# Optimization experiments

Hardware: AMD Instinct MI355X
Metric: run time of the kernel (lower is better)

## Reference

```python
import jax, jax.numpy as jnp
import numpy as np

EPS_RMS = 1e-6
Q_CLIP_MIN = 1e-5

def setup_inputs() -> dict:
    key = jax.random.key(0)
    k1, k2 = jax.random.split(key)
    x = jax.random.normal(k1, (1, 2048, 4096), dtype=jnp.float32)
    # kaiming_uniform-ish init for weight [in_features, out_features]
    fan_in = 4096
    bound = 1.0 / np.sqrt(fan_in)
    weight = jax.random.uniform(k2, (4096, 4096), dtype=jnp.float32, minval=-bound, maxval=bound)
    rms_weight = jnp.ones((4096,), dtype=jnp.float32)
    return {"x": x, "weight": weight, "rms_weight": rms_weight}

def reference(x, weight, rms_weight):
    # RMSNorm over last dim
    xn = x * jax.lax.rsqrt(jnp.mean(x * x, axis=-1, keepdims=True) + EPS_RMS) * rms_weight
    K = weight.shape[0]
    orig_shape = xn.shape
    x2 = xn.reshape(-1, K)  # [M, K]

    # per-tensor absmax int8 activation quantization
    a_scale = 127.0 / jnp.clip(jnp.max(jnp.abs(x2)), Q_CLIP_MIN)
    A_q = jnp.clip(jnp.round(x2 * a_scale), -128.0, 127.0)

    # absmean ternary weight quantization
    b_scale = 1.0 / jnp.clip(jnp.mean(jnp.abs(weight)), Q_CLIP_MIN)
    B_t = jnp.clip(jnp.round(weight * b_scale), -1.0, 1.0)

    # integer matmul + dequant: (A_q @ B_t) / (a_scale * b_scale)
    out = (A_q @ B_t) / (a_scale * b_scale)  # [M, N]
    return out.reshape(*orig_shape[:-1], weight.shape[1])
```

## Files before the change

### kernel.cpp

```cpp
#include <hip/hip_runtime.h>
#include <cstdint>

#define M_DIM 2048
#define K_DIM 4096
#define N_DIM 4096

#define BM 256
#define BN 128
#define BK 128
#define KT (K_DIM / BK)
#define A_TILE_BYTES (BM * BK)
#define B_TILE_BYTES (BN * BK)
#define TILE_BYTES (A_TILE_BYTES + B_TILE_BYTES)
#define NBUF 3
#define LDS_BYTES (NBUF * TILE_BYTES)

typedef __attribute__((ext_vector_type(4))) int i32x4;

__device__ __forceinline__ void gload_lds16(const void* g, void* l) {
  __builtin_amdgcn_global_load_lds(
      (__attribute__((address_space(1))) void*)(g),
      (__attribute__((address_space(3))) void*)(l), 16, 0, 0);
}

__global__ void fused_reduce_kernel(const float* __restrict__ x,
                                    const float* __restrict__ rw,
                                    const float* __restrict__ w,
                                    float* __restrict__ invrms,
                                    float* __restrict__ rowmax,
                                    double* __restrict__ partials) {
  const int tid = threadIdx.x;
  __shared__ double red[4];
  __shared__ float redf[4];
  __shared__ float sInv;

  if (blockIdx.x < 2048) {
    const int row = blockIdx.x;
    const float4* xr = (const float4*)(x + (size_t)row * K_DIM);
    const float4* wr = (const float4*)rw;
    float4 xv[4];
    double ss = 0.0;
#pragma unroll
    for (int i = 0; i < 4; i++) {
      xv[i] = xr[i * 256 + tid];
      ss += (double)xv[i].x * xv[i].x + (double)xv[i].y * xv[i].y +
            (double)xv[i].z * xv[i].z + (double)xv[i].w * xv[i].w;
    }
    for (int off = 32; off; off >>= 1) ss += __shfl_down(ss, off);
    if ((tid & 63) == 0) red[tid >> 6] = ss;
    __syncthreads();
    if (tid == 0) {
      double t = red[0] + red[1] + red[2] + red[3];
      sInv = (float)(1.0 / sqrt(t * (1.0 / (double)K_DIM) + 1e-6));
    }
    __syncthreads();
    const float inv = sInv;
    if (tid == 0) invrms[row] = inv;

    float amax = 0.f;
#pragma unroll
    for (int i = 0; i < 4; i++) {
      float4 wv = wr[i * 256 + tid];
      amax = fmaxf(amax, fabsf((xv[i].x * inv) * wv.x));
      amax = fmaxf(amax, fabsf((xv[i].y * inv) * wv.y));
      amax = fmaxf(amax, fabsf((xv[i].z * inv) * wv.z));
      amax = fmaxf(amax, fabsf((xv[i].w * inv) * wv.w));
    }
    for (int off = 32; off; off >>= 1) amax = fmaxf(amax, __shfl_down(amax, off));
    if ((tid & 63) == 0) redf[tid >> 6] = amax;
    __syncthreads();
    if (tid == 0)
      rowmax[row] = fmaxf(fmaxf(redf[0], redf[1]), fmaxf(redf[2], redf[3]));
  } else {
    const int bid = blockIdx.x - 2048;
    const float4* w4 = (const float4*)w;
    const size_t base = (size_t)bid * 2048;
    double s = 0.0;
#pragma unroll
    for (int i = 0; i < 8; i++) {
      float4 v = w4[base + i * 256 + tid];
      s += (double)((fabsf(v.x) + fabsf(v.y)) + (fabsf(v.z) + fabsf(v.w)));
    }
    for (int off = 32; off; off >>= 1) s += __shfl_down(s, off);
    if ((tid & 63) == 0) red[tid >> 6] = s;
    __syncthreads();
    if (tid == 0) partials[bid] = red[0] + red[1] + red[2] + red[3];
  }
}

__global__ void scales_kernel(const float* __restrict__ rowmax,
                              const double* __restrict__ partials,
                              float* __restrict__ scales) {
  const int tid = threadIdx.x;
  float m = 0.f;
  double s = 0.0;
#pragma unroll
  for (int i = 0; i < 8; i++) {
    m = fmaxf(m, rowmax[i * 256 + tid]);
    s += partials[i * 256 + tid];
  }
  for (int off = 32; off; off >>= 1) {
    m = fmaxf(m, __shfl_down(m, off));
    s += __shfl_down(s, off);
  }
  __shared__ float redf[4];
  __shared__ double red[4];
  if ((tid & 63) == 0) { redf[tid >> 6] = m; red[tid >> 6] = s; }
  __syncthreads();
  if (tid == 0) {
    float amax = fmaxf(fmaxf(redf[0], redf[1]), fmaxf(redf[2], redf[3]));
    double wsum = red[0] + red[1] + red[2] + red[3];
    float as = 127.0f / fmaxf(amax, 1e-5f);
    float mean_f = (float)(wsum * (1.0 / 16777216.0));
    float bs = 1.0f / fmaxf(mean_f, 1e-5f);
    scales[0] = as;
    scales[1] = bs;
    scales[2] = 1.0f / (as * bs);
  }
}

__global__ void fused_quant_kernel(const float* __restrict__ x,
                                   const float* __restrict__ rw,
                                   const float* __restrict__ invrms,
                                   const float* __restrict__ scales,
                                   const float* __restrict__ w,
                                   char* __restrict__ Aq,
                                   char* __restrict__ Bt) {
  const int tid = threadIdx.x;
  if (blockIdx.x < 2048) {
    const int row = blockIdx.x;
    const float inv = invrms[row];
    const float as = scales[0];
    const float4* xr = (const float4*)(x + (size_t)row * K_DIM);
    const float4* wr = (const float4*)rw;
    union { char c[16]; int4 v; } o;
#pragma unroll
    for (int i = 0; i < 4; i++) {
      float4 xv = xr[tid * 4 + i];
      float4 wv = wr[tid * 4 + i];
      float t0 = (xv.x * inv) * wv.x;
      float t1 = (xv.y * inv) * wv.y;
      float t2 = (xv.z * inv) * wv.z;
      float t3 = (xv.w * inv) * wv.w;
      o.c[i * 4 + 0] = (char)(int)fminf(fmaxf(rintf(t0 * as), -128.f), 127.f);
      o.c[i * 4 + 1] = (char)(int)fminf(fmaxf(rintf(t1 * as), -128.f), 127.f);
      o.c[i * 4 + 2] = (char)(int)fminf(fmaxf(rintf(t2 * as), -128.f), 127.f);
      o.c[i * 4 + 3] = (char)(int)fminf(fmaxf(rintf(t3 * as), -128.f), 127.f);
    }
    *(int4*)(Aq + (size_t)row * K_DIM + tid * 16) = o.v;
  } else {
    __shared__ float lds[64][68];
    const int tile = blockIdx.x - 2048;
    const int n0 = (tile & 63) * 64;
    const int k0 = (tile >> 6) * 64;
    const float bs = scales[1];
#pragma unroll
    for (int i = 0; i < 4; i++) {
      const int id = i * 256 + tid;
      const int r = id >> 4;
      const int c4 = (id & 15) * 4;
      float4 v = *(const float4*)(w + (size_t)(k0 + r) * N_DIM + n0 + c4);
      lds[c4 + 0][r] = fminf(fmaxf(rintf(v.x * bs), -1.f), 1.f);
      lds[c4 + 1][r] = fminf(fmaxf(rintf(v.y * bs), -1.f), 1.f);
      lds[c4 + 2][r] = fminf(fmaxf(rintf(v.z * bs), -1.f), 1.f);
      lds[c4 + 3][r] = fminf(fmaxf(rintf(v.w * bs), -1.f), 1.f);
    }
    __syncthreads();
    const int rn = tid >> 2;
    const int kg = (tid & 3) * 16;
    union { char c[16]; int4 v; } o;
#pragma unroll
    for (int j = 0; j < 16; j++) o.c[j] = (char)(int)lds[rn][kg + j];
    *(int4*)(Bt + (size_t)(n0 + rn) * K_DIM + k0 + kg) = o.v;
  }
}

__global__ void __launch_bounds__(512, 2)
gemm_kernel(const char* __restrict__ Aq, const char* __restrict__ Bt,
            float* __restrict__ out, const float* __restrict__ scales) {
  extern __shared__ char lds[];
  const int tid = threadIdx.x;
  const int lane = tid & 63;
  const int wave = tid >> 6;
  const int wm = wave >> 1;
  const int wn = wave & 1;
  const int brow = blockIdx.y * BM;
  const int bcol = blockIdx.x * BN;

  i32x4 acc[4][4];
#pragma unroll
  for (int m = 0; m < 4; m++)
#pragma unroll
    for (int n = 0; n < 4; n++) acc[m][n] = {0, 0, 0, 0};

  const int sRow8 = lane >> 3;
  const int srcColB = ((lane & 7) ^ sRow8) * 16;

#define STAGE_A(kt, bi, s)                                                        \
  gload_lds16(Aq + (size_t)(brow + (s)*64 + wave * 8 + sRow8) * K_DIM +           \
                  (kt)*BK + srcColB,                                              \
              lds + (bi)*TILE_BYTES + (s)*8192 + wave * 1024 + lane * 16)
#define STAGE_B(kt, bi, s)                                                        \
  gload_lds16(Bt + (size_t)(bcol + (s)*64 + wave * 8 + sRow8) * K_DIM +           \
                  (kt)*BK + srcColB,                                              \
              lds + (bi)*TILE_BYTES + A_TILE_BYTES + (s)*8192 + wave * 1024 +     \
                  lane * 16)

  STAGE_A(0, 0, 0); STAGE_A(0, 0, 1); STAGE_A(0, 0, 2); STAGE_A(0, 0, 3);
  STAGE_B(0, 0, 0); STAGE_B(0, 0, 1);
  STAGE_A(1, 1, 0); STAGE_A(1, 1, 1); STAGE_A(1, 1, 2); STAGE_A(1, 1, 3);
  STAGE_B(1, 1, 0); STAGE_B(1, 1, 1);
  asm volatile("s_waitcnt vmcnt(6)" ::: "memory");
  __builtin_amdgcn_s_barrier();

  const int aBase = (wm * 64 + (lane & 15)) * BK;
  const int bBase = (wn * 64 + (lane & 15)) * BK;
  const int swz0 = ((0 * 4 + (lane >> 4)) ^ (lane & 7)) * 16;
  const int swz1 = ((1 * 4 + (lane >> 4)) ^ (lane & 7)) * 16;

  int bi = 0;
  for (int t = 0; t < KT; ++t) {
    const char* bufA = lds + bi * TILE_BYTES;
    const char* bufB = bufA + A_TILE_BYTES;
    const int si = (bi + 2 >= NBUF) ? bi + 2 - NBUF : bi + 2;
    const bool doStage = (t + 2) < KT;

    i32x4 a0_[4], a1_[4], b0_[4], b1_[4];

#pragma unroll
    for (int s = 0; s < 2; s++) {
      a0_[s * 2 + 0] = *(const i32x4*)(bufA + aBase + s * 2048 + swz0);
      a0_[s * 2 + 1] = *(const i32x4*)(bufA + aBase + s * 2048 + swz1);
      b0_[s * 2 + 0] = *(const i32x4*)(bufB + bBase + s * 2048 + swz0);
      b0_[s * 2 + 1] = *(const i32x4*)(bufB + bBase + s * 2048 + swz1);
    }
    if (doStage) { STAGE_A(t + 2, si, 0); STAGE_A(t + 2, si, 1); }
    __builtin_amdgcn_s_barrier();
    asm volatile("s_waitcnt lgkmcnt(0)" ::: "memory");
    __builtin_amdgcn_sched_barrier(0);
    __builtin_amdgcn_s_setprio(1);
#pragma unroll
    for (int mi = 0; mi < 2; mi++)
#pragma unroll
      for (int ni = 0; ni < 2; ni++)
#pragma unroll
        for (int ks = 0; ks < 2; ks++)
          acc[mi][ni] = __builtin_amdgcn_mfma_i32_16x16x64_i8(
              a0_[mi * 2 + ks], b0_[ni * 2 + ks], acc[mi][ni], 0, 0, 0);
    __builtin_amdgcn_s_setprio(0);
    __builtin_amdgcn_s_barrier();

#pragma unroll
    for (int s = 0; s < 2; s++) {
      b1_[s * 2 + 0] = *(const i32x4*)(bufB + bBase + (s + 2) * 2048 + swz0);
      b1_[s * 2 + 1] = *(const i32x4*)(bufB + bBase + (s + 2) * 2048 + swz1);
    }
    if (doStage) { STAGE_A(t + 2, si, 2); STAGE_A(t + 2, si, 3); }
    __builtin_amdgcn_s_barrier();
    asm volatile("s_waitcnt lgkmcnt(0)" ::: "memory");
    __builtin_amdgcn_sched_barrier(0);
    __builtin_amdgcn_s_setprio(1);
#pragma unroll
    for (int mi = 0; mi < 2; mi++)
#pragma unroll
      for (int ni = 0; ni < 2; ni++)
#pragma unroll
        for (int ks = 0; ks < 2; ks++)
          acc[mi][ni + 2] = __builtin_amdgcn_mfma_i32_16x16x64_i8(
              a0_[mi * 2 + ks], b1_[ni * 2 + ks], acc[mi][ni + 2], 0, 0, 0);
    __builtin_amdgcn_s_setprio(0);
    __builtin_amdgcn_s_barrier();

#pragma unroll
    for (int s = 0; s < 2; s++) {
      a1_[s * 2 + 0] = *(const i32x4*)(bufA + aBase + (s + 2) * 2048 + swz0);
      a1_[s * 2 + 1] = *(const i32x4*)(bufA + aBase + (s + 2) * 2048 + swz1);
    }
    if (doStage) { STAGE_B(t + 2, si, 0); STAGE_B(t + 2, si, 1); }
    __builtin_amdgcn_s_barrier();
    asm volatile("s_waitcnt lgkmcnt(0)" ::: "memory");
    __builtin_amdgcn_sched_barrier(0);
    __builtin_amdgcn_s_setprio(1);
#pragma unroll
    for (int mi = 0; mi < 2; mi++)
#pragma unroll
      for (int ni = 0; ni < 2; ni++)
#pragma unroll
        for (int ks = 0; ks < 2; ks++)
          acc[mi + 2][ni] = __builtin_amdgcn_mfma_i32_16x16x64_i8(
              a1_[mi * 2 + ks], b0_[ni * 2 + ks], acc[mi + 2][ni], 0, 0, 0);
    __builtin_amdgcn_s_setprio(0);
    __builtin_amdgcn_s_barrier();

    __builtin_amdgcn_s_setprio(1);
#pragma unroll
    for (int mi = 0; mi < 2; mi++)
#pragma unroll
      for (int ni = 0; ni < 2; ni++)
#pragma unroll
        for (int ks = 0; ks < 2; ks++)
          acc[mi + 2][ni + 2] = __builtin_amdgcn_mfma_i32_16x16x64_i8(
              a1_[mi * 2 + ks], b1_[ni * 2 + ks], acc[mi + 2][ni + 2], 0, 0, 0);
    __builtin_amdgcn_s_setprio(0);
    if (t < KT - 1) {
      asm volatile("s_waitcnt vmcnt(6)" ::: "memory");
    } else {
      asm volatile("s_waitcnt vmcnt(0)" ::: "memory");
    }
    __builtin_amdgcn_s_barrier();

    bi = (bi + 1 >= NBUF) ? 0 : bi + 1;
  }
#undef STAGE_A
#undef STAGE_B

  const float dq = scales[2];
#pragma unroll
  for (int m = 0; m < 4; m++) {
#pragma unroll
    for (int n = 0; n < 4; n++) {
      const int row = wm * 64 + m * 16 + (lane >> 4) * 4;
      const int col = wn * 64 + n * 16 + (lane & 15);
#pragma unroll
      for (int j = 0; j < 4; j++) {
        out[(size_t)(brow + row + j) * N_DIM + bcol + col] = (float)acc[m][n][j] * dq;
      }
    }
  }
}

extern "C" void kernel_launch(void* const* d_in, const int* in_sizes, int n_in,
                              void* d_out, int out_size, void* d_ws, size_t ws_size,
                              hipStream_t stream) {
  const float* x      = (const float*)d_in[0];
  const float* weight = (const float*)d_in[1];
  const float* rms_w  = (const float*)d_in[2];
  float* out = (float*)d_out;

  uint8_t* ws = (uint8_t*)d_ws;
  float* scales    = (float*)(ws + 0);
  float* invrms    = (float*)(ws + 64);
  float* rowmax    = (float*)(ws + 64 + 8192);
  double* partials = (double*)(ws + 64 + 16384);
  char* Aq = (char*)(ws + 65536);
  char* Bt = (char*)(ws + 65536 + (size_t)M_DIM * K_DIM);

  (void)hipFuncSetAttribute((const void*)gemm_kernel,
                            hipFuncAttributeMaxDynamicSharedMemorySize, LDS_BYTES);

  fused_reduce_kernel<<<4096, 256, 0, stream>>>(x, rms_w, weight, invrms, rowmax, partials);
  scales_kernel<<<1, 256, 0, stream>>>(rowmax, partials, scales);
  fused_quant_kernel<<<6144, 256, 0, stream>>>(x, rms_w, invrms, scales, weight, Aq, Bt);
  gemm_kernel<<<dim3(N_DIM / BN, M_DIM / BM), 512, LDS_BYTES, stream>>>(Aq, Bt, out, scales);
}
```

Before: 77.32 us.

## Cut per-iteration barriers to one and overlap LDS reads with MFMA via partial lgkmcnt waits

Restructures the int8 GEMM main loop so each K-step has a single vmcnt wait plus workgroup barrier at the top, replacing the many intra-iteration s_barriers. LDS fragment loads for the next MFMA group are issued before the current group runs, and partial lgkmcnt(4) waits let MFMAs start while later loads are still in flight. Global-to-LDS staging is regrouped as 3+3 issues instead of 2+2+2. The aim is to remove barrier stalls and expose more load/compute overlap. The cost is tighter reliance on the triple-buffer distance for correctness, since fewer barriers separate staging writes from reads of other buffers.

```diff
diff --git a/kernel.cpp b/kernel.cpp
--- a/kernel.cpp
+++ b/kernel.cpp
@@ -210,8 +210,6 @@
   STAGE_B(0, 0, 0); STAGE_B(0, 0, 1);
   STAGE_A(1, 1, 0); STAGE_A(1, 1, 1); STAGE_A(1, 1, 2); STAGE_A(1, 1, 3);
   STAGE_B(1, 1, 0); STAGE_B(1, 1, 1);
-  asm volatile("s_waitcnt vmcnt(6)" ::: "memory");
-  __builtin_amdgcn_s_barrier();
 
   const int aBase = (wm * 64 + (lane & 15)) * BK;
   const int bBase = (wn * 64 + (lane & 15)) * BK;
@@ -220,23 +218,37 @@
 
   int bi = 0;
   for (int t = 0; t < KT; ++t) {
+    if (t < KT - 1) {
+      asm volatile("s_waitcnt vmcnt(6)" ::: "memory");
+    } else {
+      asm volatile("s_waitcnt vmcnt(0)" ::: "memory");
+    }
+    __builtin_amdgcn_s_barrier();
+    __builtin_amdgcn_sched_barrier(0);
+
     const char* bufA = lds + bi * TILE_BYTES;
     const char* bufB = bufA + A_TILE_BYTES;
     const int si = (bi + 2 >= NBUF) ? bi + 2 - NBUF : bi + 2;
     const bool doStage = (t + 2) < KT;
 
-    i32x4 a0_[4], a1_[4], b0_[4], b1_[4];
+    i32x4 a0[4], a1[4], b0[4], b1[4];
 
 #pragma unroll
     for (int s = 0; s < 2; s++) {
-      a0_[s * 2 + 0] = *(const i32x4*)(bufA + aBase + s * 2048 + swz0);
-      a0_[s * 2 + 1] = *(const i32x4*)(bufA + aBase + s * 2048 + swz1);
-      b0_[s * 2 + 0] = *(const i32x4*)(bufB + bBase + s * 2048 + swz0);
-      b0_[s * 2 + 1] = *(const i32x4*)(bufB + bBase + s * 2048 + swz1);
-    }
-    if (doStage) { STAGE_A(t + 2, si, 0); STAGE_A(t + 2, si, 1); }
-    __builtin_amdgcn_s_barrier();
-    asm volatile("s_waitcnt lgkmcnt(0)" ::: "memory");
+      a0[s * 2 + 0] = *(const i32x4*)(bufA + aBase + s * 2048 + swz0);
+      a0[s * 2 + 1] = *(const i32x4*)(bufA + aBase + s * 2048 + swz1);
+      b0[s * 2 + 0] = *(const i32x4*)(bufB + bBase + s * 2048 + swz0);
+      b0[s * 2 + 1] = *(const i32x4*)(bufB + bBase + s * 2048 + swz1);
+    }
+    if (doStage) { STAGE_A(t + 2, si, 0); STAGE_A(t + 2, si, 1); STAGE_A(t + 2, si, 2); }
+    __builtin_amdgcn_sched_barrier(0);
+
+#pragma unroll
+    for (int s = 0; s < 2; s++) {
+      b1[s * 2 + 0] = *(const i32x4*)(bufB + bBase + (s + 2) * 2048 + swz0);
+      b1[s * 2 + 1] = *(const i32x4*)(bufB + bBase + (s + 2) * 2048 + swz1);
+    }
+    asm volatile("s_waitcnt lgkmcnt(4)" ::: "memory");
     __builtin_amdgcn_sched_barrier(0);
     __builtin_amdgcn_s_setprio(1);
 #pragma unroll
@@ -246,18 +258,16 @@
 #pragma unroll
         for (int ks = 0; ks < 2; ks++)
           acc[mi][ni] = __builtin_amdgcn_mfma_i32_16x16x64_i8(
-              a0_[mi * 2 + ks], b0_[ni * 2 + ks], acc[mi][ni], 0, 0, 0);
+              a0[mi * 2 + ks], b0[ni * 2 + ks], acc[mi][ni], 0, 0, 0);
     __builtin_amdgcn_s_setprio(0);
-    __builtin_amdgcn_s_barrier();
 
 #pragma unroll
     for (int s = 0; s < 2; s++) {
-      b1_[s * 2 + 0] = *(const i32x4*)(bufB + bBase + (s + 2) * 2048 + swz0);
-      b1_[s * 2 + 1] = *(const i32x4*)(bufB + bBase + (s + 2) * 2048 + swz1);
-    }
-    if (doStage) { STAGE_A(t + 2, si, 2); STAGE_A(t + 2, si, 3); }
-    __builtin_amdgcn_s_barrier();
-    asm volatile("s_waitcnt lgkmcnt(0)" ::: "memory");
+      a1[s * 2 + 0] = *(const i32x4*)(bufA + aBase + (s + 2) * 2048 + swz0);
+      a1[s * 2 + 1] = *(const i32x4*)(bufA + aBase + (s + 2) * 2048 + swz1);
+    }
+    if (doStage) { STAGE_A(t + 2, si, 3); STAGE_B(t + 2, si, 0); STAGE_B(t + 2, si, 1); }
+    asm volatile("s_waitcnt lgkmcnt(4)" ::: "memory");
     __builtin_amdgcn_sched_barrier(0);
     __builtin_amdgcn_s_setprio(1);
 #pragma unroll
@@ -267,17 +277,9 @@
 #pragma unroll
         for (int ks = 0; ks < 2; ks++)
           acc[mi][ni + 2] = __builtin_amdgcn_mfma_i32_16x16x64_i8(
-              a0_[mi * 2 + ks], b1_[ni * 2 + ks], acc[mi][ni + 2], 0, 0, 0);
+              a0[mi * 2 + ks], b1[ni * 2 + ks], acc[mi][ni + 2], 0, 0, 0);
     __builtin_amdgcn_s_setprio(0);
-    __builtin_amdgcn_s_barrier();
-
-#pragma unroll
-    for (int s = 0; s < 2; s++) {
-      a1_[s * 2 + 0] = *(const i32x4*)(bufA + aBase + (s + 2) * 2048 + swz0);
-      a1_[s * 2 + 1] = *(const i32x4*)(bufA + aBase + (s + 2) * 2048 + swz1);
-    }
-    if (doStage) { STAGE_B(t + 2, si, 0); STAGE_B(t + 2, si, 1); }
-    __builtin_amdgcn_s_barrier();
+
     asm volatile("s_waitcnt lgkmcnt(0)" ::: "memory");
     __builtin_amdgcn_sched_barrier(0);
     __builtin_amdgcn_s_setprio(1);
@@ -288,11 +290,7 @@
 #pragma unroll
         for (int ks = 0; ks < 2; ks++)
           acc[mi + 2][ni] = __builtin_amdgcn_mfma_i32_16x16x64_i8(
-              a1_[mi * 2 + ks], b0_[ni * 2 + ks], acc[mi + 2][ni], 0, 0, 0);
-    __builtin_amdgcn_s_setprio(0);
-    __builtin_amdgcn_s_barrier();
-
-    __builtin_amdgcn_s_setprio(1);
+              a1[mi * 2 + ks], b0[ni * 2 + ks], acc[mi + 2][ni], 0, 0, 0);
 #pragma unroll
     for (int mi = 0; mi < 2; mi++)
 #pragma unroll
@@ -300,14 +298,8 @@
 #pragma unroll
         for (int ks = 0; ks < 2; ks++)
           acc[mi + 2][ni + 2] = __builtin_amdgcn_mfma_i32_16x16x64_i8(
-              a1_[mi * 2 + ks], b1_[ni * 2 + ks], acc[mi + 2][ni + 2], 0, 0, 0);
+              a1[mi * 2 + ks], b1[ni * 2 + ks], acc[mi + 2][ni + 2], 0, 0, 0);
     __builtin_amdgcn_s_setprio(0);
-    if (t < KT - 1) {
-      asm volatile("s_waitcnt vmcnt(6)" ::: "memory");
-    } else {
-      asm volatile("s_waitcnt vmcnt(0)" ::: "memory");
-    }
-    __builtin_amdgcn_s_barrier();
 
     bi = (bi + 1 >= NBUF) ? 0 : bi + 1;
   }
```

After: 75.40 us. 1.03x faster.
